# Kernel tuning notes

Measured on AMD Instinct MI355X. Metric: run time of the kernel, lower is better.

## Reference

```python
import jax, jax.numpy as jnp
import numpy as np

V, E, C, L, H, I = 50304, 512, 256, 6, 8, 1024
D = C // H            # head_dim = 32
ROT = int(D * 0.25)   # rotary_ndims = 8
B, S = 4, 1024


def _ln(x, w, b, eps=1e-5):
    m = x.mean(-1, keepdims=True)
    v = ((x - m) ** 2).mean(-1, keepdims=True)
    return (x - m) * jax.lax.rsqrt(v + eps) * w + b


def _apply_rope(x, cos, sin):
    # x: [B,S,H,D]; GPT-NeoX partial rotary on first ROT dims
    xr, xp = x[..., :ROT], x[..., ROT:]
    half = ROT // 2
    xrh = jnp.concatenate([-xr[..., half:], xr[..., :half]], -1)
    return jnp.concatenate([xr * cos + xrh * sin, xp], -1)


def setup_inputs() -> dict:
    key = jax.random.key(0)
    ks = jax.random.split(key, 16)
    std = 0.02
    inp = {
        'input_ids': jax.random.randint(ks[0], (B, S), 0, V),
        'prev_context': jnp.zeros((B, C), jnp.float32),
        'embed_w': jax.random.normal(ks[1], (V, E)) * std,
        'en_w': jnp.ones((E,)), 'en_b': jnp.zeros((E,)),
        # ContextBlock: Linear(context_dim+embed_dim -> context_dim) + GELU + LayerNorm
        'ctx_w': jax.random.normal(ks[2], (C, C + E)) * std,
        'ctx_b': jnp.zeros((C,)),
        'cn_w': jnp.ones((C,)), 'cn_b': jnp.zeros((C,)),
        # stacked per-layer Pythia params [L, ...]
        'ln1_w': jnp.ones((L, C)), 'ln1_b': jnp.zeros((L, C)),
        'ln2_w': jnp.ones((L, C)), 'ln2_b': jnp.zeros((L, C)),
        'qkv_w': jax.random.normal(ks[3], (L, 3 * C, C)) * std,
        'qkv_b': jnp.zeros((L, 3 * C)),
        'ao_w': jax.random.normal(ks[4], (L, C, C)) * std,
        'ao_b': jnp.zeros((L, C)),
        'fc1_w': jax.random.normal(ks[5], (L, I, C)) * std,
        'fc1_b': jnp.zeros((L, I)),
        'fc2_w': jax.random.normal(ks[6], (L, C, I)) * std,
        'fc2_b': jnp.zeros((L, C)),
        'fln_w': jnp.ones((C,)), 'fln_b': jnp.zeros((C,)),
        'out_w': jax.random.normal(ks[7], (V, C)) * std,
    }
    return inp


def reference(input_ids, prev_context, embed_w, en_w, en_b, ctx_w, ctx_b, cn_w, cn_b,
              ln1_w, ln1_b, ln2_w, ln2_b, qkv_w, qkv_b, ao_w, ao_b,
              fc1_w, fc1_b, fc2_w, fc2_b, fln_w, fln_b, out_w):
    b, s = input_ids.shape
    tok = _ln(embed_w[input_ids], en_w, en_b)                 # [B,S,E]

    # sequential context recurrence (scan == the per-token Python loop)
    def step(ctx, emb_t):
        h = jnp.concatenate([ctx, emb_t], -1) @ ctx_w.T + ctx_b
        ctx_new = _ln(jax.nn.gelu(h), cn_w, cn_b)
        return ctx_new, ctx_new
    _, hs = jax.lax.scan(step, prev_context, tok.transpose(1, 0, 2))
    x = hs.transpose(1, 0, 2)                                 # [B,S,C]

    pos = jnp.arange(s)
    inv = 1.0 / (10000.0 ** (jnp.arange(0, ROT, 2, dtype=jnp.float32) / ROT))
    ang = pos[:, None] * inv                                  # [S, ROT/2]
    cos = jnp.tile(jnp.cos(ang), (1, 2))[None, :, None, :]
    sin = jnp.tile(jnp.sin(ang), (1, 2))[None, :, None, :]
    causal = jnp.tril(jnp.ones((s, s), bool))

    for l in range(L):
        # parallel residual Pythia/GPT-NeoX layer
        a_in = _ln(x, ln1_w[l], ln1_b[l])
        qkv = jnp.einsum('bsc,oc->bso', a_in, qkv_w[l]) + qkv_b[l]
        q, k, v = [t.reshape(b, s, H, D) for t in jnp.split(qkv, 3, -1)]
        q = _apply_rope(q, cos, sin)
        k = _apply_rope(k, cos, sin)
        sc = jnp.einsum('bqhd,bkhd->bhqk', q, k) / jnp.sqrt(jnp.float32(D))
        sc = jnp.where(causal, sc, jnp.float32(-1e9))
        p = jax.nn.softmax(sc, -1)
        o = jnp.einsum('bhqk,bkhd->bqhd', p, v).reshape(b, s, C)
        attn = o @ ao_w[l].T + ao_b[l]
        m_in = _ln(x, ln2_w[l], ln2_b[l])
        mlp = jax.nn.gelu(m_in @ fc1_w[l].T + fc1_b[l]) @ fc2_w[l].T + fc2_b[l]
        x = x + attn + mlp

    x = _ln(x, fln_w, fln_b)
    logits = jnp.einsum('bsc,vc->bsv', x, out_w)              # [B,S,V]
    return logits
```

## Files before the change

kernel.cpp:

```cpp
#include <hip/hip_runtime.h>

typedef __bf16 bf16x8 __attribute__((ext_vector_type(8)));
typedef float  f32x4  __attribute__((ext_vector_type(4)));
typedef unsigned uint32x4 __attribute__((ext_vector_type(4)));

#define DEV __device__ __forceinline__

DEV ushort f2bf(float f) {
  unsigned u = __builtin_bit_cast(unsigned, f);
  u += 0x7FFFu + ((u >> 16) & 1u);
  return (ushort)(u >> 16);
}
DEV float bf2f(ushort u) { return __builtin_bit_cast(float, ((unsigned)u) << 16); }
DEV unsigned pk2(ushort a, ushort b) { return (unsigned)a | ((unsigned)b << 16); }

DEV f32x4 mfma16(bf16x8 a, bf16x8 b, f32x4 c) {
  return __builtin_amdgcn_mfma_f32_16x16x32_bf16(a, b, c, 0, 0, 0);
}

DEV float gelu_f(float x) {
  float u = 0.7978845608028654f * (x + 0.044715f * x * x * x);
  return x / (1.f + __expf(-2.f * u));
}

#define SEQ  1024
#define NBAT 4
#define CDIM 256
#define EDIM 512
#define NLAY 6
#define NHEAD 8
#define HDIM 32
#define IDIM 1024
#define NVOC 50304
#define NROWS (NBAT * SEQ)

__global__ __launch_bounds__(256) void cvt_k(const float* __restrict__ src,
                                             ushort* __restrict__ dst, int n4) {
  int i = blockIdx.x * blockDim.x + threadIdx.x;
  int stride = gridDim.x * blockDim.x;
  for (; i < n4; i += stride) {
    float4 f = ((const float4*)src)[i];
    ushort4 u; u.x = f2bf(f.x); u.y = f2bf(f.y); u.z = f2bf(f.z); u.w = f2bf(f.w);
    ((ushort4*)dst)[i] = u;
  }
}

__global__ __launch_bounds__(64) void embed_ln_k(const int* __restrict__ ids,
                                                 const float* __restrict__ ew,
                                                 const float* __restrict__ w,
                                                 const float* __restrict__ b,
                                                 ushort* __restrict__ tok) {
  int m = blockIdx.x, t = threadIdx.x;
  const float* row = ew + (size_t)ids[m] * EDIM;
  float4 v0 = *(const float4*)(row + t * 8);
  float4 v1 = *(const float4*)(row + t * 8 + 4);
  float sm = v0.x + v0.y + v0.z + v0.w + v1.x + v1.y + v1.z + v1.w;
  float sq = v0.x*v0.x + v0.y*v0.y + v0.z*v0.z + v0.w*v0.w
           + v1.x*v1.x + v1.y*v1.y + v1.z*v1.z + v1.w*v1.w;
#pragma unroll
  for (int msk = 1; msk <= 32; msk <<= 1) { sm += __shfl_xor(sm, msk); sq += __shfl_xor(sq, msk); }
  float mean = sm * (1.f / EDIM);
  float var  = sq * (1.f / EDIM) - mean * mean;
  float inv  = rsqrtf(var + 1e-5f);
  float4 w0 = *(const float4*)(w + t * 8), w1 = *(const float4*)(w + t * 8 + 4);
  float4 b0 = *(const float4*)(b + t * 8), b1 = *(const float4*)(b + t * 8 + 4);
  ushort4 u0, u1;
  u0.x = f2bf((v0.x - mean) * inv * w0.x + b0.x);
  u0.y = f2bf((v0.y - mean) * inv * w0.y + b0.y);
  u0.z = f2bf((v0.z - mean) * inv * w0.z + b0.z);
  u0.w = f2bf((v0.w - mean) * inv * w0.w + b0.w);
  u1.x = f2bf((v1.x - mean) * inv * w1.x + b1.x);
  u1.y = f2bf((v1.y - mean) * inv * w1.y + b1.y);
  u1.z = f2bf((v1.z - mean) * inv * w1.z + b1.z);
  u1.w = f2bf((v1.w - mean) * inv * w1.w + b1.w);
  *(ushort4*)(tok + (size_t)m * EDIM + t * 8)     = u0;
  *(ushort4*)(tok + (size_t)m * EDIM + t * 8 + 4) = u1;
}

template <bool DUAL>
__global__ __launch_bounds__(256) void ln_k(const float* __restrict__ x,
                                            const float* __restrict__ w1, const float* __restrict__ b1,
                                            const float* __restrict__ w2, const float* __restrict__ b2,
                                            ushort* __restrict__ o1, ushort* __restrict__ o2) {
  int wave = threadIdx.x >> 6, t = threadIdx.x & 63;
  int m = blockIdx.x * 4 + wave;
  const float* row = x + (size_t)m * CDIM;
  float4 v = *(const float4*)(row + t * 4);
  float sm = v.x + v.y + v.z + v.w;
  float sq = v.x*v.x + v.y*v.y + v.z*v.z + v.w*v.w;
#pragma unroll
  for (int msk = 1; msk <= 32; msk <<= 1) { sm += __shfl_xor(sm, msk); sq += __shfl_xor(sq, msk); }
  float mean = sm * (1.f / CDIM);
  float var  = sq * (1.f / CDIM) - mean * mean;
  float inv  = rsqrtf(var + 1e-5f);
  float n0 = (v.x - mean) * inv, n1 = (v.y - mean) * inv, n2 = (v.z - mean) * inv, n3 = (v.w - mean) * inv;
  {
    float4 wv = *(const float4*)(w1 + t * 4), bv = *(const float4*)(b1 + t * 4);
    ushort4 u; u.x = f2bf(n0*wv.x+bv.x); u.y = f2bf(n1*wv.y+bv.y); u.z = f2bf(n2*wv.z+bv.z); u.w = f2bf(n3*wv.w+bv.w);
    *(ushort4*)(o1 + (size_t)m * CDIM + t * 4) = u;
  }
  if constexpr (DUAL) {
    float4 wv = *(const float4*)(w2 + t * 4), bv = *(const float4*)(b2 + t * 4);
    ushort4 u; u.x = f2bf(n0*wv.x+bv.x); u.y = f2bf(n1*wv.y+bv.y); u.z = f2bf(n2*wv.z+bv.z); u.w = f2bf(n3*wv.w+bv.w);
    *(ushort4*)(o2 + (size_t)m * CDIM + t * 4) = u;
  }
}

enum { GF_BIAS = 1, GF_GELU = 2, GF_ACC = 4, GF_BF16O = 8, GF_WF32 = 16 };

template <int FLAGS>
__global__ __launch_bounds__(256) void gemm_k(const ushort* __restrict__ A, int lda,
                                              const void* __restrict__ Wv, int ldw,
                                              const float* __restrict__ bias,
                                              void* __restrict__ C, int ldc, int K) {
  __shared__ __attribute__((aligned(16))) ushort lsA[128 * 32];
  __shared__ __attribute__((aligned(16))) ushort lsB[128 * 32];
  const int tid = threadIdx.x, lane = tid & 63, wave = tid >> 6;
  const int wm = wave >> 1, wn = wave & 1;
  const int row0 = blockIdx.x * 128, col0 = blockIdx.y * 128;
  const int l15 = lane & 15, koff = (lane >> 4) * 8;

  f32x4 acc[4][4] = {};
  for (int k0 = 0; k0 < K; k0 += 32) {
    __syncthreads();
#pragma unroll
    for (int p = 0; p < 2; ++p) {
      int c = tid + p * 256;
      int r = c >> 2, k8 = (c & 3) * 8;
      *(uint4*)(&lsA[c * 8]) = *(const uint4*)(A + (size_t)(row0 + r) * lda + k0 + k8);
      if constexpr (FLAGS & GF_WF32) {
        const float* gw = (const float*)Wv + (size_t)(col0 + r) * ldw + k0 + k8;
        float4 f0 = *(const float4*)gw, f1 = *(const float4*)(gw + 4);
        uint4 vw;
        vw.x = pk2(f2bf(f0.x), f2bf(f0.y)); vw.y = pk2(f2bf(f0.z), f2bf(f0.w));
        vw.z = pk2(f2bf(f1.x), f2bf(f1.y)); vw.w = pk2(f2bf(f1.z), f2bf(f1.w));
        *(uint4*)(&lsB[c * 8]) = vw;
      } else {
        *(uint4*)(&lsB[c * 8]) = *(const uint4*)((const ushort*)Wv + (size_t)(col0 + r) * ldw + k0 + k8);
      }
    }
    __syncthreads();
    bf16x8 af[4], bfr[4];
#pragma unroll
    for (int mt = 0; mt < 4; ++mt)
      af[mt] = __builtin_bit_cast(bf16x8, *(const uint4*)(&lsA[(wm * 64 + mt * 16 + l15) * 32 + koff]));
#pragma unroll
    for (int nt = 0; nt < 4; ++nt)
      bfr[nt] = __builtin_bit_cast(bf16x8, *(const uint4*)(&lsB[(wn * 64 + nt * 16 + l15) * 32 + koff]));
#pragma unroll
    for (int mt = 0; mt < 4; ++mt)
#pragma unroll
      for (int nt = 0; nt < 4; ++nt)
        acc[mt][nt] = mfma16(af[mt], bfr[nt], acc[mt][nt]);
  }
#pragma unroll
  for (int mt = 0; mt < 4; ++mt) {
#pragma unroll
    for (int nt = 0; nt < 4; ++nt) {
      int col = col0 + wn * 64 + nt * 16 + l15;
      float bv = (FLAGS & GF_BIAS) ? bias[col] : 0.f;
      int rowb = row0 + wm * 64 + mt * 16 + (lane >> 4) * 4;
#pragma unroll
      for (int r = 0; r < 4; ++r) {
        float v = acc[mt][nt][r] + bv;
        if constexpr (FLAGS & GF_GELU) v = gelu_f(v);
        size_t off = (size_t)(rowb + r) * ldc + col;
        if constexpr (FLAGS & GF_ACC)        ((float*)C)[off] += v;
        else if constexpr (FLAGS & GF_BF16O) ((ushort*)C)[off] = f2bf(v);
        else                                 ((float*)C)[off] = v;
      }
    }
  }
}

template <int FLAGS>
__global__ __launch_bounds__(256) void gemm64_k(const ushort* __restrict__ A, int lda,
                                                const void* __restrict__ Wv, int ldw,
                                                const float* __restrict__ bias,
                                                void* __restrict__ C, int ldc, int K) {
  __shared__ __attribute__((aligned(16))) ushort lsA[64 * 32];
  __shared__ __attribute__((aligned(16))) ushort lsB[64 * 32];
  const int tid = threadIdx.x, lane = tid & 63, wave = tid >> 6;
  const int row0 = blockIdx.x * 64, col0 = blockIdx.y * 64;
  const int l15 = lane & 15, lhi = lane >> 4, koff = lhi * 8;

  f32x4 acc[4] = {};
  for (int k0 = 0; k0 < K; k0 += 32) {
    __syncthreads();
    {
      int r = tid >> 2, k8 = (tid & 3) * 8;
      *(uint4*)(&lsA[tid * 8]) = *(const uint4*)(A + (size_t)(row0 + r) * lda + k0 + k8);
      if constexpr (FLAGS & GF_WF32) {
        const float* gw = (const float*)Wv + (size_t)(col0 + r) * ldw + k0 + k8;
        float4 f0 = *(const float4*)gw, f1 = *(const float4*)(gw + 4);
        uint4 vw;
        vw.x = pk2(f2bf(f0.x), f2bf(f0.y)); vw.y = pk2(f2bf(f0.z), f2bf(f0.w));
        vw.z = pk2(f2bf(f1.x), f2bf(f1.y)); vw.w = pk2(f2bf(f1.z), f2bf(f1.w));
        *(uint4*)(&lsB[tid * 8]) = vw;
      } else {
        *(uint4*)(&lsB[tid * 8]) = *(const uint4*)((const ushort*)Wv + (size_t)(col0 + r) * ldw + k0 + k8);
      }
    }
    __syncthreads();
    bf16x8 af = __builtin_bit_cast(bf16x8, *(const uint4*)(&lsA[(wave * 16 + l15) * 32 + koff]));
#pragma unroll
    for (int nt = 0; nt < 4; ++nt) {
      bf16x8 bfr = __builtin_bit_cast(bf16x8, *(const uint4*)(&lsB[(nt * 16 + l15) * 32 + koff]));
      acc[nt] = mfma16(af, bfr, acc[nt]);
    }
  }
#pragma unroll
  for (int nt = 0; nt < 4; ++nt) {
    int col = col0 + nt * 16 + l15;
    float bv = (FLAGS & GF_BIAS) ? bias[col] : 0.f;
    int rowb = row0 + wave * 16 + lhi * 4;
#pragma unroll
    for (int r = 0; r < 4; ++r) {
      float v = acc[nt][r] + bv;
      if constexpr (FLAGS & GF_GELU) v = gelu_f(v);
      size_t off = (size_t)(rowb + r) * ldc + col;
      if constexpr (FLAGS & GF_ACC)        ((float*)C)[off] += v;
      else if constexpr (FLAGS & GF_BF16O) ((ushort*)C)[off] = f2bf(v);
      else                                 ((float*)C)[off] = v;
    }
  }
}

__global__ __launch_bounds__(512, 2) void scan_k(const float* __restrict__ ctx_w,
                                                 const float* __restrict__ prev_ctx,
                                                 const float* __restrict__ P,
                                                 const float* __restrict__ cn_w,
                                                 const float* __restrict__ cn_b,
                                                 float* __restrict__ x) {
  __shared__ __attribute__((aligned(16))) ushort g_lds[2][4 * 288];
  __shared__ __attribute__((aligned(16))) float  part_lds[2][4][8][2];
  const int tid = threadIdx.x, lane = tid & 63, wave = tid >> 6;
  const int l15 = lane & 15, lhi = lane >> 4;
  const int bb = l15 & 3;
  const int ss = l15 >> 2;
  const int mt = ss & 1, rp = ss >> 1;
  const int c0 = wave * 32 + mt * 16 + lhi * 4 + rp * 2;

  float2 wv  = *(const float2*)(cn_w + c0);
  float2 bv2 = *(const float2*)(cn_b + c0);
  float s1v0 = 0.f, s1v1 = 0.f, c1v0 = 0.f, c1v1 = 0.f;
#pragma unroll 1
  for (int kk = 0; kk < CDIM; kk += 4) {
    float4 wk = *(const float4*)(cn_w + kk);
    float4 bk = *(const float4*)(cn_b + kk);
    float4 W0 = *(const float4*)(ctx_w + (size_t)c0 * 768 + kk);
    float4 W1 = *(const float4*)(ctx_w + (size_t)(c0 + 1) * 768 + kk);
    s1v0 += W0.x*wk.x + W0.y*wk.y + W0.z*wk.z + W0.w*wk.w;
    c1v0 += W0.x*bk.x + W0.y*bk.y + W0.z*bk.z + W0.w*bk.w;
    s1v1 += W1.x*wk.x + W1.y*wk.y + W1.z*wk.z + W1.w*wk.w;
    c1v1 += W1.x*bk.x + W1.y*bk.y + W1.z*bk.z + W1.w*bk.w;
  }

  {
    float2 c2 = *(const float2*)(prev_ctx + bb * CDIM + c0);
    ushort2 u; u.x = f2bf(c2.x); u.y = f2bf(c2.y);
    *(ushort2*)&g_lds[0][bb * 288 + c0] = u;
  }

  uint32x4 wfu[2][8];
#pragma unroll
  for (int m2 = 0; m2 < 2; ++m2)
#pragma unroll
    for (int kt = 0; kt < 8; ++kt) {
      const float* s = ctx_w + (size_t)(wave * 32 + m2 * 16 + l15) * 768 + kt * 32 + lhi * 8;
      float4 f0 = *(const float4*)s, f1 = *(const float4*)(s + 4);
      uint32x4 vw;
      vw.x = pk2(f2bf(f0.x), f2bf(f0.y)); vw.y = pk2(f2bf(f0.z), f2bf(f0.w));
      vw.z = pk2(f2bf(f1.x), f2bf(f1.y)); vw.w = pk2(f2bf(f1.z), f2bf(f1.w));
      wfu[m2][kt] = vw;
    }
  float2 pf  = *(const float2*)(P + ((size_t)bb * SEQ + 0) * CDIM + c0);
  float2 pn1 = *(const float2*)(P + ((size_t)bb * SEQ + 1) * CDIM + c0);
  float2 pn2 = *(const float2*)(P + ((size_t)bb * SEQ + 2) * CDIM + c0);
  __syncthreads();

  float gr[2];
  {
    uint32x4 bfr[8];
#pragma unroll
    for (int kt = 0; kt < 8; ++kt)
      bfr[kt] = *(const uint32x4*)(&g_lds[0][bb * 288 + kt * 32 + lhi * 8]);
    f32x4 acc[2] = {};
#pragma unroll
    for (int m2 = 0; m2 < 2; ++m2)
#pragma unroll
      for (int kt = 0; kt < 8; ++kt)
        acc[m2] = mfma16(__builtin_bit_cast(bf16x8, wfu[m2][kt]),
                         __builtin_bit_cast(bf16x8, bfr[kt]), acc[m2]);
    f32x4 av = (mt == 0) ? acc[0] : acc[1];
    gr[0] = gelu_f(av[rp * 2]     + pf.x);
    gr[1] = gelu_f(av[rp * 2 + 1] + pf.y);
  }

#pragma unroll
  for (int m2 = 0; m2 < 2; ++m2)
#pragma unroll
    for (int kt = 0; kt < 8; ++kt) {
      int k = kt * 32 + lhi * 8;
      const float* s = ctx_w + (size_t)(wave * 32 + m2 * 16 + l15) * 768 + k;
      float4 f0 = *(const float4*)s, f1 = *(const float4*)(s + 4);
      float4 w0 = *(const float4*)(cn_w + k), w1 = *(const float4*)(cn_w + k + 4);
      uint32x4 vw;
      vw.x = pk2(f2bf(f0.x * w0.x), f2bf(f0.y * w0.y));
      vw.y = pk2(f2bf(f0.z * w0.z), f2bf(f0.w * w0.w));
      vw.z = pk2(f2bf(f1.x * w1.x), f2bf(f1.y * w1.y));
      vw.w = pk2(f2bf(f1.z * w1.z), f2bf(f1.w * w1.w));
      wfu[m2][kt] = vw;
    }
#pragma unroll
  for (int m2 = 0; m2 < 2; ++m2)
#pragma unroll
    for (int kt = 0; kt < 8; ++kt)
      asm volatile("" : "+v"(wfu[m2][kt]));
  pf = pn1; pn1 = pn2;
  pn2 = *(const float2*)(P + ((size_t)bb * SEQ + 3) * CDIM + c0);
  __syncthreads();

  {
    ushort2 u; u.x = f2bf(gr[0]); u.y = f2bf(gr[1]);
    *(ushort2*)&g_lds[0][bb * 288 + c0] = u;
    float lsm = gr[0] + gr[1];
    float lsq = gr[0]*gr[0] + gr[1]*gr[1];
    lsm += __shfl_xor(lsm, 4);  lsq += __shfl_xor(lsq, 4);
    lsm += __shfl_xor(lsm, 8);  lsq += __shfl_xor(lsq, 8);
    lsm += __shfl_xor(lsm, 16); lsq += __shfl_xor(lsq, 16);
    lsm += __shfl_xor(lsm, 32); lsq += __shfl_xor(lsq, 32);
    if (ss == 0 && lhi == 0) {
      float2 pq; pq.x = lsm; pq.y = lsq;
      *(float2*)&part_lds[0][l15][wave][0] = pq;
    }
  }
  __syncthreads();

  for (int t = 0; t < SEQ; ++t) {
    const int cur = t & 1, nxt = cur ^ 1;
    int tp = (t + 4 < SEQ) ? t + 4 : SEQ - 1;
    float2 pl = *(const float2*)(P + ((size_t)bb * SEQ + tp) * CDIM + c0);

    uint32x4 bfr[8];
#pragma unroll
    for (int kt = 0; kt < 8; ++kt)
      bfr[kt] = *(const uint32x4*)(&g_lds[cur][bb * 288 + kt * 32 + lhi * 8]);
    const float4* pp = (const float4*)&part_lds[cur][bb][0][0];
    float4 qa = pp[0], qb = pp[1], qc = pp[2], qd = pp[3];

    f32x4 accA[2] = {}, accB[2] = {};
#pragma unroll
    for (int m2 = 0; m2 < 2; ++m2) {
      accA[m2] = mfma16(__builtin_bit_cast(bf16x8, wfu[m2][0]), __builtin_bit_cast(bf16x8, bfr[0]), accA[m2]);
      accB[m2] = mfma16(__builtin_bit_cast(bf16x8, wfu[m2][4]), __builtin_bit_cast(bf16x8, bfr[4]), accB[m2]);
      accA[m2] = mfma16(__builtin_bit_cast(bf16x8, wfu[m2][1]), __builtin_bit_cast(bf16x8, bfr[1]), accA[m2]);
      accB[m2] = mfma16(__builtin_bit_cast(bf16x8, wfu[m2][5]), __builtin_bit_cast(bf16x8, bfr[5]), accB[m2]);
      accA[m2] = mfma16(__builtin_bit_cast(bf16x8, wfu[m2][2]), __builtin_bit_cast(bf16x8, bfr[2]), accA[m2]);
      accB[m2] = mfma16(__builtin_bit_cast(bf16x8, wfu[m2][6]), __builtin_bit_cast(bf16x8, bfr[6]), accB[m2]);
      accA[m2] = mfma16(__builtin_bit_cast(bf16x8, wfu[m2][3]), __builtin_bit_cast(bf16x8, bfr[3]), accA[m2]);
      accB[m2] = mfma16(__builtin_bit_cast(bf16x8, wfu[m2][7]), __builtin_bit_cast(bf16x8, bfr[7]), accB[m2]);
    }

    float sm = (qa.x + qa.z) + (qb.x + qb.z) + (qc.x + qc.z) + (qd.x + qd.z);
    float sq = (qa.y + qa.w) + (qb.y + qb.w) + (qc.y + qc.w) + (qd.y + qd.w);
    float mu  = sm * (1.f / CDIM);
    float inv = rsqrtf(sq * (1.f / CDIM) - mu * mu + 1e-5f);
    float invmu = inv * mu;

    float2 y;
    y.x = wv.x * (inv * gr[0] - invmu) + bv2.x;
    y.y = wv.y * (inv * gr[1] - invmu) + bv2.y;
    *(float2*)(x + ((size_t)bb * SEQ + t) * CDIM + c0) = y;

    f32x4 avA = (mt == 0) ? accA[0] : accA[1];
    f32x4 avB = (mt == 0) ? accB[0] : accB[1];
    float a0 = avA[rp * 2]     + avB[rp * 2];
    float a1 = avA[rp * 2 + 1] + avB[rp * 2 + 1];
    gr[0] = gelu_f(inv * a0 - invmu * s1v0 + c1v0 + pf.x);
    gr[1] = gelu_f(inv * a1 - invmu * s1v1 + c1v1 + pf.y);
    {
      ushort2 u; u.x = f2bf(gr[0]); u.y = f2bf(gr[1]);
      *(ushort2*)&g_lds[nxt][bb * 288 + c0] = u;
    }
    float lsm = gr[0] + gr[1];
    float lsq = gr[0]*gr[0] + gr[1]*gr[1];
    lsm += __shfl_xor(lsm, 4);  lsq += __shfl_xor(lsq, 4);
    lsm += __shfl_xor(lsm, 8);  lsq += __shfl_xor(lsq, 8);
    lsm += __shfl_xor(lsm, 16); lsq += __shfl_xor(lsq, 16);
    lsm += __shfl_xor(lsm, 32); lsq += __shfl_xor(lsq, 32);
    if (ss == 0 && lhi == 0) {
      float2 pq; pq.x = lsm; pq.y = lsq;
      *(float2*)&part_lds[nxt][l15][wave][0] = pq;
    }
    pf = pn1; pn1 = pn2; pn2 = pl;
    asm volatile("s_waitcnt lgkmcnt(0)" ::: "memory");
    __builtin_amdgcn_s_barrier();
    __builtin_amdgcn_sched_barrier(0);
  }
}

__global__ __launch_bounds__(256) void rope_k(const ushort* __restrict__ qkv,
                                              ushort* __restrict__ Qo,
                                              ushort* __restrict__ Ko,
                                              ushort* __restrict__ Vt) {
  int m = blockIdx.x;
  int b = m >> 10, s = m & 1023;
  int t = threadIdx.x;
  int h = t >> 5, d = t & 31;
  const ushort* row = qkv + (size_t)m * 768;
  float q = bf2f(row[h * 32 + d]);
  float k = bf2f(row[256 + h * 32 + d]);
  float v = bf2f(row[512 + h * 32 + d]);
  if (d < 8) {
    int prt = (d < 4) ? d + 4 : d - 4;
    float sgn = (d < 4) ? -1.f : 1.f;
    float qp = sgn * bf2f(row[h * 32 + prt]);
    float kp = sgn * bf2f(row[256 + h * 32 + prt]);
    int j = d & 3;
    const float invs[4] = {1.f, 0.1f, 0.01f, 0.001f};
    float ang = (float)s * invs[j];
    float c, sn;
    __sincosf(ang, &sn, &c);
    q = q * c + qp * sn;
    k = k * c + kp * sn;
  }
  size_t bh = (size_t)(b * NHEAD + h);
  Qo[(bh * SEQ + s) * HDIM + d] = f2bf(q);
  Ko[(bh * SEQ + s) * HDIM + d] = f2bf(k);
  Vt[bh * HDIM * SEQ + (size_t)d * SEQ + s] = f2bf(v);
}

__global__ __launch_bounds__(256) void attn_k(const ushort* __restrict__ Q,
                                              const ushort* __restrict__ K,
                                              const ushort* __restrict__ VT,
                                              ushort* __restrict__ O) {
  __shared__ __attribute__((aligned(16))) ushort Plds[4 * 16 * 32];
  const int tid = threadIdx.x, lane = tid & 63, wave = tid >> 6;
  const int bh = blockIdx.y;
  const int qtile = blockIdx.x * 4 + wave;
  const int q0 = qtile * 16;
  const int l15 = lane & 15, lhi = lane >> 4;
  const float scale = 0.17677669529663689f;

  bf16x8 qa = __builtin_bit_cast(bf16x8,
      *(const uint4*)(Q + ((size_t)bh * SEQ + q0 + l15) * HDIM + lhi * 8));
  const ushort* Kb = K + (size_t)bh * SEQ * HDIM;
  const ushort* Vb = VT + (size_t)bh * HDIM * SEQ;
  ushort* Pw = &Plds[wave * 512];

  f32x4 o0 = {}, o1 = {};
  float lacc[4] = {};

  for (int kt = 0; kt <= qtile; kt += 2) {
    const bool t2 = (kt + 1 <= qtile);
    f32x4 z = {};
    bf16x8 kf0 = __builtin_bit_cast(bf16x8, *(const uint4*)(Kb + (size_t)(kt * 16 + l15) * HDIM + lhi * 8));
    f32x4 s0 = mfma16(qa, kf0, z);
    f32x4 s1 = {};
    if (t2) {
      bf16x8 kf1 = __builtin_bit_cast(bf16x8, *(const uint4*)(Kb + (size_t)((kt + 1) * 16 + l15) * HDIM + lhi * 8));
      s1 = mfma16(qa, kf1, z);
    }
    float p0[4], p1[4];
#pragma unroll
    for (int r = 0; r < 4; ++r) {
      int qr = q0 + lhi * 4 + r;
      int kc0 = kt * 16 + l15;
      p0[r] = (kc0 <= qr) ? __expf(s0[r] * scale) : 0.f;
      p1[r] = (t2 && kc0 + 16 <= qr) ? __expf(s1[r] * scale) : 0.f;
      lacc[r] += p0[r] + p1[r];
    }
#pragma unroll
    for (int r = 0; r < 4; ++r) {
      Pw[(lhi * 4 + r) * 32 + l15]      = f2bf(p0[r]);
      Pw[(lhi * 4 + r) * 32 + 16 + l15] = f2bf(p1[r]);
    }
    bf16x8 pa  = __builtin_bit_cast(bf16x8, *(const uint4*)(&Pw[l15 * 32 + lhi * 8]));
    bf16x8 v0f = __builtin_bit_cast(bf16x8, *(const uint4*)(Vb + (size_t)l15 * SEQ + kt * 16 + lhi * 8));
    bf16x8 v1f = __builtin_bit_cast(bf16x8, *(const uint4*)(Vb + (size_t)(16 + l15) * SEQ + kt * 16 + lhi * 8));
    o0 = mfma16(pa, v0f, o0);
    o1 = mfma16(pa, v1f, o1);
  }
#pragma unroll
  for (int msk = 1; msk <= 8; msk <<= 1)
#pragma unroll
    for (int r = 0; r < 4; ++r) lacc[r] += __shfl_xor(lacc[r], msk);

  const int b = bh >> 3, h = bh & 7;
#pragma unroll
  for (int r = 0; r < 4; ++r) {
    float inv = 1.f / lacc[r];
    int qr = q0 + lhi * 4 + r;
    size_t base = ((size_t)(b * SEQ + qr)) * CDIM + h * HDIM;
    O[base + l15]      = f2bf(o0[r] * inv);
    O[base + 16 + l15] = f2bf(o1[r] * inv);
  }
}

static size_t ws_take(size_t& o, size_t bytes) {
  size_t r = o;
  o += (bytes + 255) & ~(size_t)255;
  return r;
}

extern "C" void kernel_launch(void* const* d_in, const int* in_sizes, int n_in,
                              void* d_out, int out_size, void* d_ws, size_t ws_size,
                              hipStream_t stream) {
  (void)in_sizes; (void)n_in; (void)out_size; (void)ws_size;
  const int*   input_ids = (const int*)  d_in[0];
  const float* prev_ctx  = (const float*)d_in[1];
  const float* embed_w   = (const float*)d_in[2];
  const float* en_w      = (const float*)d_in[3];
  const float* en_b      = (const float*)d_in[4];
  const float* ctx_w     = (const float*)d_in[5];
  const float* ctx_b     = (const float*)d_in[6];
  const float* cn_w      = (const float*)d_in[7];
  const float* cn_b      = (const float*)d_in[8];
  const float* ln1_w     = (const float*)d_in[9];
  const float* ln1_b     = (const float*)d_in[10];
  const float* ln2_w     = (const float*)d_in[11];
  const float* ln2_b     = (const float*)d_in[12];
  const float* qkv_w     = (const float*)d_in[13];
  const float* qkv_b     = (const float*)d_in[14];
  const float* ao_w      = (const float*)d_in[15];
  const float* ao_b      = (const float*)d_in[16];
  const float* fc1_w     = (const float*)d_in[17];
  const float* fc1_b     = (const float*)d_in[18];
  const float* fc2_w     = (const float*)d_in[19];
  const float* fc2_b     = (const float*)d_in[20];
  const float* fln_w     = (const float*)d_in[21];
  const float* fln_b     = (const float*)d_in[22];
  const float* out_w     = (const float*)d_in[23];
  float* logits = (float*)d_out;

  char* ws = (char*)d_ws;
  size_t o = 0;
  ushort* WB_OUT = (ushort*)(ws + ws_take(o, (size_t)NVOC * CDIM * 2));
  ushort* TOK    = (ushort*)(ws + ws_take(o, (size_t)NROWS * EDIM * 2));
  float*  PBUF   = (float*) (ws + ws_take(o, (size_t)NROWS * CDIM * 4));
  float*  XBUF   = (float*) (ws + ws_take(o, (size_t)NROWS * CDIM * 4));
  ushort* AIN    = (ushort*)(ws + ws_take(o, (size_t)NROWS * CDIM * 2));
  ushort* MIN    = (ushort*)(ws + ws_take(o, (size_t)NROWS * CDIM * 2));
  ushort* QKVB   = (ushort*)(ws + ws_take(o, (size_t)NROWS * 768 * 2));
  ushort* QB     = (ushort*)(ws + ws_take(o, (size_t)NROWS * CDIM * 2));
  ushort* KB     = (ushort*)(ws + ws_take(o, (size_t)NROWS * CDIM * 2));
  ushort* VTB    = (ushort*)(ws + ws_take(o, (size_t)NROWS * CDIM * 2));
  ushort* OB     = (ushort*)(ws + ws_take(o, (size_t)NROWS * CDIM * 2));
  ushort* TBUF   = (ushort*)(ws + ws_take(o, (size_t)NROWS * IDIM * 2));
  ushort* XLN    = (ushort*)(ws + ws_take(o, (size_t)NROWS * CDIM * 2));

  cvt_k<<<dim3(2048), dim3(256), 0, stream>>>(out_w, WB_OUT, NVOC * CDIM / 4);
  embed_ln_k<<<dim3(NROWS), dim3(64), 0, stream>>>(input_ids, embed_w, en_w, en_b, TOK);
  gemm64_k<GF_BIAS | GF_WF32><<<dim3(64, 4), dim3(256), 0, stream>>>(
      TOK, EDIM, (const void*)(ctx_w + 256), 768, ctx_b, (void*)PBUF, CDIM, EDIM);
  scan_k<<<dim3(1), dim3(512), 0, stream>>>(ctx_w, prev_ctx, PBUF, cn_w, cn_b, XBUF);

  for (int l = 0; l < NLAY; ++l) {
    ln_k<true><<<dim3(NROWS / 4), dim3(256), 0, stream>>>(
        XBUF, ln1_w + l * CDIM, ln1_b + l * CDIM, ln2_w + l * CDIM, ln2_b + l * CDIM, AIN, MIN);
    gemm64_k<GF_BIAS | GF_BF16O | GF_WF32><<<dim3(64, 12), dim3(256), 0, stream>>>(
        AIN, CDIM, (const void*)(qkv_w + (size_t)l * 768 * CDIM), CDIM,
        qkv_b + l * 768, (void*)QKVB, 768, CDIM);
    rope_k<<<dim3(NROWS), dim3(256), 0, stream>>>(QKVB, QB, KB, VTB);
    attn_k<<<dim3(16, 32), dim3(256), 0, stream>>>(QB, KB, VTB, OB);
    gemm64_k<GF_BIAS | GF_ACC | GF_WF32><<<dim3(64, 4), dim3(256), 0, stream>>>(
        OB, CDIM, (const void*)(ao_w + (size_t)l * CDIM * CDIM), CDIM,
        ao_b + l * CDIM, (void*)XBUF, CDIM, CDIM);
    gemm64_k<GF_BIAS | GF_GELU | GF_BF16O | GF_WF32><<<dim3(64, 16), dim3(256), 0, stream>>>(
        MIN, CDIM, (const void*)(fc1_w + (size_t)l * IDIM * CDIM), CDIM,
        fc1_b + l * IDIM, (void*)TBUF, IDIM, CDIM);
    gemm64_k<GF_BIAS | GF_ACC | GF_WF32><<<dim3(64, 4), dim3(256), 0, stream>>>(
        TBUF, IDIM, (const void*)(fc2_w + (size_t)l * CDIM * IDIM), IDIM,
        fc2_b + l * CDIM, (void*)XBUF, CDIM, IDIM);
  }

  ln_k<false><<<dim3(NROWS / 4), dim3(256), 0, stream>>>(
      XBUF, fln_w, fln_b, nullptr, nullptr, XLN, nullptr);
  gemm_k<0><<<dim3(32, 393), dim3(256), 0, stream>>>(
      XLN, CDIM, (const void*)WB_OUT, CDIM, nullptr, (void*)logits, NVOC, CDIM);
}
```

Measured before the change: 2.020 ms.

## Fuse RoPE into QKV GEMM, merge attn-out and FC2 GEMMs, restructure scan

Three independent changes. RoPE is folded into the QKV GEMM epilogue, using a lane shuffle to fetch the rotary partner, so the intermediate QKV buffer and the separate rope kernel go away. The attention-output and FC2 projections become one dual-K GEMM that accumulates into the residual once, removing a launch and one read-modify-write of X per layer. The sequential scan kernel drops from 8 to 4 waves, with each lane owning 4 columns, and is unrolled by 4 so the prefetch registers rotate statically; the aim is shorter per-step barrier and reduction cost on the serial critical path, at the price of more MFMA work per wave.

Result: faster. 1.805 ms (-10.6%).

```diff
diff --git a/kernel.cpp b/kernel.cpp
--- a/kernel.cpp
+++ b/kernel.cpp
@@ -226,83 +226,199 @@
   }
 }
 
-__global__ __launch_bounds__(512, 2) void scan_k(const float* __restrict__ ctx_w,
+__global__ __launch_bounds__(256) void qkvrope_k(const ushort* __restrict__ A,
+                                                 const float* __restrict__ W,
+                                                 const float* __restrict__ bias,
+                                                 ushort* __restrict__ Qo,
+                                                 ushort* __restrict__ Ko,
+                                                 ushort* __restrict__ Vt) {
+  __shared__ __attribute__((aligned(16))) ushort lsA[64 * 32];
+  __shared__ __attribute__((aligned(16))) ushort lsB[64 * 32];
+  const int tid = threadIdx.x, lane = tid & 63, wave = tid >> 6;
+  const int row0 = blockIdx.x * 64, col0 = blockIdx.y * 64;
+  const int l15 = lane & 15, lhi = lane >> 4, koff = lhi * 8;
+
+  f32x4 acc[4] = {};
+  for (int k0 = 0; k0 < CDIM; k0 += 32) {
+    __syncthreads();
+    {
+      int r = tid >> 2, k8 = (tid & 3) * 8;
+      *(uint4*)(&lsA[tid * 8]) = *(const uint4*)(A + (size_t)(row0 + r) * CDIM + k0 + k8);
+      const float* gw = W + (size_t)(col0 + r) * CDIM + k0 + k8;
+      float4 f0 = *(const float4*)gw, f1 = *(const float4*)(gw + 4);
+      uint4 vw;
+      vw.x = pk2(f2bf(f0.x), f2bf(f0.y)); vw.y = pk2(f2bf(f0.z), f2bf(f0.w));
+      vw.z = pk2(f2bf(f1.x), f2bf(f1.y)); vw.w = pk2(f2bf(f1.z), f2bf(f1.w));
+      *(uint4*)(&lsB[tid * 8]) = vw;
+    }
+    __syncthreads();
+    bf16x8 af = __builtin_bit_cast(bf16x8, *(const uint4*)(&lsA[(wave * 16 + l15) * 32 + koff]));
+#pragma unroll
+    for (int nt = 0; nt < 4; ++nt) {
+      bf16x8 bfr = __builtin_bit_cast(bf16x8, *(const uint4*)(&lsB[(nt * 16 + l15) * 32 + koff]));
+      acc[nt] = mfma16(af, bfr, acc[nt]);
+    }
+  }
+  const int rowb = row0 + wave * 16 + lhi * 4;
+  const int b = rowb >> 10, s0 = rowb & 1023;
+#pragma unroll
+  for (int nt = 0; nt < 4; ++nt) {
+    int c = col0 + nt * 16 + l15;
+    int which = c >> 8;
+    int h = (c >> 5) & 7;
+    int d = c & 31;
+    size_t bh = (size_t)(b * NHEAD + h);
+    float bv = bias[c];
+    float val[4], part[4];
+#pragma unroll
+    for (int r = 0; r < 4; ++r) val[r] = acc[nt][r] + bv;
+#pragma unroll
+    for (int r = 0; r < 4; ++r) part[r] = __shfl_xor(val[r], 4);
+    if (d < 8 && which < 2) {
+      float sgn = (d < 4) ? -1.f : 1.f;
+      int j = d & 3;
+      float invp = (j == 0) ? 1.f : (j == 1) ? 0.1f : (j == 2) ? 0.01f : 0.001f;
+#pragma unroll
+      for (int r = 0; r < 4; ++r) {
+        float ang = (float)(s0 + r) * invp;
+        float cs, sn;
+        __sincosf(ang, &sn, &cs);
+        val[r] = val[r] * cs + sgn * part[r] * sn;
+      }
+    }
+    if (which == 2) {
+      ushort4 u; u.x = f2bf(val[0]); u.y = f2bf(val[1]); u.z = f2bf(val[2]); u.w = f2bf(val[3]);
+      *(ushort4*)(Vt + bh * HDIM * SEQ + (size_t)d * SEQ + s0) = u;
+    } else {
+      ushort* dst = (which == 0) ? Qo : Ko;
+#pragma unroll
+      for (int r = 0; r < 4; ++r)
+        dst[(bh * SEQ + s0 + r) * HDIM + d] = f2bf(val[r]);
+    }
+  }
+}
+
+__global__ __launch_bounds__(256) void gemm64_dual_k(const ushort* __restrict__ A1, int lda1,
+                                                     const float* __restrict__ W1, int ldw1, int K1,
+                                                     const ushort* __restrict__ A2, int lda2,
+                                                     const float* __restrict__ W2, int ldw2, int K2,
+                                                     const float* __restrict__ b1,
+                                                     const float* __restrict__ b2,
+                                                     float* __restrict__ C, int ldc) {
+  __shared__ __attribute__((aligned(16))) ushort lsA[64 * 32];
+  __shared__ __attribute__((aligned(16))) ushort lsB[64 * 32];
+  const int tid = threadIdx.x, lane = tid & 63, wave = tid >> 6;
+  const int row0 = blockIdx.x * 64, col0 = blockIdx.y * 64;
+  const int l15 = lane & 15, lhi = lane >> 4, koff = lhi * 8;
+
+  f32x4 acc[4] = {};
+  for (int k0 = 0; k0 < K1 + K2; k0 += 32) {
+    __syncthreads();
+    {
+      int r = tid >> 2, k8 = (tid & 3) * 8;
+      const ushort* Ap; const float* Wp; int kk;
+      if (k0 < K1) { Ap = A1 + (size_t)(row0 + r) * lda1; Wp = W1 + (size_t)(col0 + r) * ldw1; kk = k0 + k8; }
+      else         { Ap = A2 + (size_t)(row0 + r) * lda2; Wp = W2 + (size_t)(col0 + r) * ldw2; kk = k0 - K1 + k8; }
+      *(uint4*)(&lsA[tid * 8]) = *(const uint4*)(Ap + kk);
+      float4 f0 = *(const float4*)(Wp + kk), f1 = *(const float4*)(Wp + kk + 4);
+      uint4 vw;
+      vw.x = pk2(f2bf(f0.x), f2bf(f0.y)); vw.y = pk2(f2bf(f0.z), f2bf(f0.w));
+      vw.z = pk2(f2bf(f1.x), f2bf(f1.y)); vw.w = pk2(f2bf(f1.z), f2bf(f1.w));
+      *(uint4*)(&lsB[tid * 8]) = vw;
+    }
+    __syncthreads();
+    bf16x8 af = __builtin_bit_cast(bf16x8, *(const uint4*)(&lsA[(wave * 16 + l15) * 32 + koff]));
+#pragma unroll
+    for (int nt = 0; nt < 4; ++nt) {
+      bf16x8 bfr = __builtin_bit_cast(bf16x8, *(const uint4*)(&lsB[(nt * 16 + l15) * 32 + koff]));
+      acc[nt] = mfma16(af, bfr, acc[nt]);
+    }
+  }
+#pragma unroll
+  for (int nt = 0; nt < 4; ++nt) {
+    int col = col0 + nt * 16 + l15;
+    float bv = b1[col] + b2[col];
+    int rowb = row0 + wave * 16 + lhi * 4;
+#pragma unroll
+    for (int r = 0; r < 4; ++r)
+      C[(size_t)(rowb + r) * ldc + col] += acc[nt][r] + bv;
+  }
+}
+
+__global__ __launch_bounds__(256, 1) void scan_k(const float* __restrict__ ctx_w,
                                                  const float* __restrict__ prev_ctx,
                                                  const float* __restrict__ P,
                                                  const float* __restrict__ cn_w,
                                                  const float* __restrict__ cn_b,
                                                  float* __restrict__ x) {
   __shared__ __attribute__((aligned(16))) ushort g_lds[2][4 * 288];
-  __shared__ __attribute__((aligned(16))) float  part_lds[2][4][8][2];
+  __shared__ __attribute__((aligned(16))) float  part_lds[2][4][4][2];
   const int tid = threadIdx.x, lane = tid & 63, wave = tid >> 6;
   const int l15 = lane & 15, lhi = lane >> 4;
   const int bb = l15 & 3;
   const int ss = l15 >> 2;
-  const int mt = ss & 1, rp = ss >> 1;
-  const int c0 = wave * 32 + mt * 16 + lhi * 4 + rp * 2;
-
-  float2 wv  = *(const float2*)(cn_w + c0);
-  float2 bv2 = *(const float2*)(cn_b + c0);
-  float s1v0 = 0.f, s1v1 = 0.f, c1v0 = 0.f, c1v1 = 0.f;
+  const int ccol = wave * 64 + ss * 16 + lhi * 4;
+
+  float4 wv  = *(const float4*)(cn_w + ccol);
+  float4 bvv = *(const float4*)(cn_b + ccol);
+  float s1v[4] = {}, c1v[4] = {};
 #pragma unroll 1
   for (int kk = 0; kk < CDIM; kk += 4) {
     float4 wk = *(const float4*)(cn_w + kk);
     float4 bk = *(const float4*)(cn_b + kk);
-    float4 W0 = *(const float4*)(ctx_w + (size_t)c0 * 768 + kk);
-    float4 W1 = *(const float4*)(ctx_w + (size_t)(c0 + 1) * 768 + kk);
-    s1v0 += W0.x*wk.x + W0.y*wk.y + W0.z*wk.z + W0.w*wk.w;
-    c1v0 += W0.x*bk.x + W0.y*bk.y + W0.z*bk.z + W0.w*bk.w;
-    s1v1 += W1.x*wk.x + W1.y*wk.y + W1.z*wk.z + W1.w*wk.w;
-    c1v1 += W1.x*bk.x + W1.y*bk.y + W1.z*bk.z + W1.w*bk.w;
+#pragma unroll
+    for (int j = 0; j < 4; ++j) {
+      float4 Wr = *(const float4*)(ctx_w + (size_t)(ccol + j) * 768 + kk);
+      s1v[j] += Wr.x * wk.x + Wr.y * wk.y + Wr.z * wk.z + Wr.w * wk.w;
+      c1v[j] += Wr.x * bk.x + Wr.y * bk.y + Wr.z * bk.z + Wr.w * bk.w;
+    }
   }
 
   {
-    float2 c2 = *(const float2*)(prev_ctx + bb * CDIM + c0);
-    ushort2 u; u.x = f2bf(c2.x); u.y = f2bf(c2.y);
-    *(ushort2*)&g_lds[0][bb * 288 + c0] = u;
-  }
-
-  uint32x4 wfu[2][8];
-#pragma unroll
-  for (int m2 = 0; m2 < 2; ++m2)
+    float4 c4 = *(const float4*)(prev_ctx + bb * CDIM + ccol);
+    ushort4 u; u.x = f2bf(c4.x); u.y = f2bf(c4.y); u.z = f2bf(c4.z); u.w = f2bf(c4.w);
+    *(ushort4*)&g_lds[0][bb * 288 + ccol] = u;
+  }
+
+  uint32x4 wfu[4][8];
+#pragma unroll
+  for (int mt = 0; mt < 4; ++mt)
 #pragma unroll
     for (int kt = 0; kt < 8; ++kt) {
-      const float* s = ctx_w + (size_t)(wave * 32 + m2 * 16 + l15) * 768 + kt * 32 + lhi * 8;
+      const float* s = ctx_w + (size_t)(wave * 64 + mt * 16 + l15) * 768 + kt * 32 + lhi * 8;
       float4 f0 = *(const float4*)s, f1 = *(const float4*)(s + 4);
       uint32x4 vw;
       vw.x = pk2(f2bf(f0.x), f2bf(f0.y)); vw.y = pk2(f2bf(f0.z), f2bf(f0.w));
       vw.z = pk2(f2bf(f1.x), f2bf(f1.y)); vw.w = pk2(f2bf(f1.z), f2bf(f1.w));
-      wfu[m2][kt] = vw;
-    }
-  float2 pf  = *(const float2*)(P + ((size_t)bb * SEQ + 0) * CDIM + c0);
-  float2 pn1 = *(const float2*)(P + ((size_t)bb * SEQ + 1) * CDIM + c0);
-  float2 pn2 = *(const float2*)(P + ((size_t)bb * SEQ + 2) * CDIM + c0);
+      wfu[mt][kt] = vw;
+    }
+  float4 pf = *(const float4*)(P + ((size_t)bb * SEQ + 0) * CDIM + ccol);
   __syncthreads();
 
-  float gr[2];
+  float gr[4];
   {
     uint32x4 bfr[8];
 #pragma unroll
     for (int kt = 0; kt < 8; ++kt)
       bfr[kt] = *(const uint32x4*)(&g_lds[0][bb * 288 + kt * 32 + lhi * 8]);
-    f32x4 acc[2] = {};
-#pragma unroll
-    for (int m2 = 0; m2 < 2; ++m2)
+    f32x4 acc[4] = {};
+#pragma unroll
+    for (int mt = 0; mt < 4; ++mt)
 #pragma unroll
       for (int kt = 0; kt < 8; ++kt)
-        acc[m2] = mfma16(__builtin_bit_cast(bf16x8, wfu[m2][kt]),
-                         __builtin_bit_cast(bf16x8, bfr[kt]), acc[m2]);
-    f32x4 av = (mt == 0) ? acc[0] : acc[1];
-    gr[0] = gelu_f(av[rp * 2]     + pf.x);
-    gr[1] = gelu_f(av[rp * 2 + 1] + pf.y);
-  }
-
-#pragma unroll
-  for (int m2 = 0; m2 < 2; ++m2)
+        acc[mt] = mfma16(__builtin_bit_cast(bf16x8, wfu[mt][kt]),
+                         __builtin_bit_cast(bf16x8, bfr[kt]), acc[mt]);
+    f32x4 av = (ss == 0) ? acc[0] : (ss == 1) ? acc[1] : (ss == 2) ? acc[2] : acc[3];
+    gr[0] = gelu_f(av[0] + pf.x); gr[1] = gelu_f(av[1] + pf.y);
+    gr[2] = gelu_f(av[2] + pf.z); gr[3] = gelu_f(av[3] + pf.w);
+  }
+
+#pragma unroll
+  for (int mt = 0; mt < 4; ++mt)
 #pragma unroll
     for (int kt = 0; kt < 8; ++kt) {
       int k = kt * 32 + lhi * 8;
-      const float* s = ctx_w + (size_t)(wave * 32 + m2 * 16 + l15) * 768 + k;
+      const float* s = ctx_w + (size_t)(wave * 64 + mt * 16 + l15) * 768 + k;
       float4 f0 = *(const float4*)s, f1 = *(const float4*)(s + 4);
       float4 w0 = *(const float4*)(cn_w + k), w1 = *(const float4*)(cn_w + k + 4);
       uint32x4 vw;
@@ -310,125 +426,103 @@
       vw.y = pk2(f2bf(f0.z * w0.z), f2bf(f0.w * w0.w));
       vw.z = pk2(f2bf(f1.x * w1.x), f2bf(f1.y * w1.y));
       vw.w = pk2(f2bf(f1.z * w1.z), f2bf(f1.w * w1.w));
-      wfu[m2][kt] = vw;
-    }
-#pragma unroll
-  for (int m2 = 0; m2 < 2; ++m2)
+      wfu[mt][kt] = vw;
+    }
+#pragma unroll
+  for (int mt = 0; mt < 4; ++mt)
 #pragma unroll
     for (int kt = 0; kt < 8; ++kt)
-      asm volatile("" : "+v"(wfu[m2][kt]));
-  pf = pn1; pn1 = pn2;
-  pn2 = *(const float2*)(P + ((size_t)bb * SEQ + 3) * CDIM + c0);
+      asm volatile("" : "+v"(wfu[mt][kt]));
+
+  float4 ps0, ps1, ps2, ps3;
+  ps1 = *(const float4*)(P + ((size_t)bb * SEQ + 1) * CDIM + ccol);
+  ps2 = *(const float4*)(P + ((size_t)bb * SEQ + 2) * CDIM + ccol);
+  ps3 = *(const float4*)(P + ((size_t)bb * SEQ + 3) * CDIM + ccol);
+  ps0 = ps3;
   __syncthreads();
 
   {
-    ushort2 u; u.x = f2bf(gr[0]); u.y = f2bf(gr[1]);
-    *(ushort2*)&g_lds[0][bb * 288 + c0] = u;
-    float lsm = gr[0] + gr[1];
-    float lsq = gr[0]*gr[0] + gr[1]*gr[1];
+    ushort4 u; u.x = f2bf(gr[0]); u.y = f2bf(gr[1]); u.z = f2bf(gr[2]); u.w = f2bf(gr[3]);
+    *(ushort4*)&g_lds[0][bb * 288 + ccol] = u;
+    float lsm = gr[0] + gr[1] + gr[2] + gr[3];
+    float lsq = gr[0]*gr[0] + gr[1]*gr[1] + gr[2]*gr[2] + gr[3]*gr[3];
     lsm += __shfl_xor(lsm, 4);  lsq += __shfl_xor(lsq, 4);
     lsm += __shfl_xor(lsm, 8);  lsq += __shfl_xor(lsq, 8);
     lsm += __shfl_xor(lsm, 16); lsq += __shfl_xor(lsq, 16);
     lsm += __shfl_xor(lsm, 32); lsq += __shfl_xor(lsq, 32);
     if (ss == 0 && lhi == 0) {
-      float2 pq; pq.x = lsm; pq.y = lsq;
-      *(float2*)&part_lds[0][l15][wave][0] = pq;
+      part_lds[0][bb][wave][0] = lsm;
+      part_lds[0][bb][wave][1] = lsq;
     }
   }
   __syncthreads();
 
-  for (int t = 0; t < SEQ; ++t) {
-    const int cur = t & 1, nxt = cur ^ 1;
-    int tp = (t + 4 < SEQ) ? t + 4 : SEQ - 1;
-    float2 pl = *(const float2*)(P + ((size_t)bb * SEQ + tp) * CDIM + c0);
-
-    uint32x4 bfr[8];
-#pragma unroll
-    for (int kt = 0; kt < 8; ++kt)
-      bfr[kt] = *(const uint32x4*)(&g_lds[cur][bb * 288 + kt * 32 + lhi * 8]);
-    const float4* pp = (const float4*)&part_lds[cur][bb][0][0];
-    float4 qa = pp[0], qb = pp[1], qc = pp[2], qd = pp[3];
-
-    f32x4 accA[2] = {}, accB[2] = {};
-#pragma unroll
-    for (int m2 = 0; m2 < 2; ++m2) {
-      accA[m2] = mfma16(__builtin_bit_cast(bf16x8, wfu[m2][0]), __builtin_bit_cast(bf16x8, bfr[0]), accA[m2]);
-      accB[m2] = mfma16(__builtin_bit_cast(bf16x8, wfu[m2][4]), __builtin_bit_cast(bf16x8, bfr[4]), accB[m2]);
-      accA[m2] = mfma16(__builtin_bit_cast(bf16x8, wfu[m2][1]), __builtin_bit_cast(bf16x8, bfr[1]), accA[m2]);
-      accB[m2] = mfma16(__builtin_bit_cast(bf16x8, wfu[m2][5]), __builtin_bit_cast(bf16x8, bfr[5]), accB[m2]);
-      accA[m2] = mfma16(__builtin_bit_cast(bf16x8, wfu[m2][2]), __builtin_bit_cast(bf16x8, bfr[2]), accA[m2]);
-      accB[m2] = mfma16(__builtin_bit_cast(bf16x8, wfu[m2][6]), __builtin_bit_cast(bf16x8, bfr[6]), accB[m2]);
-      accA[m2] = mfma16(__builtin_bit_cast(bf16x8, wfu[m2][3]), __builtin_bit_cast(bf16x8, bfr[3]), accA[m2]);
-      accB[m2] = mfma16(__builtin_bit_cast(bf16x8, wfu[m2][7]), __builtin_bit_cast(bf16x8, bfr[7]), accB[m2]);
-    }
-
-    float sm = (qa.x + qa.z) + (qb.x + qb.z) + (qc.x + qc.z) + (qd.x + qd.z);
-    float sq = (qa.y + qa.w) + (qb.y + qb.w) + (qc.y + qc.w) + (qd.y + qd.w);
-    float mu  = sm * (1.f / CDIM);
-    float inv = rsqrtf(sq * (1.f / CDIM) - mu * mu + 1e-5f);
-    float invmu = inv * mu;
-
-    float2 y;
-    y.x = wv.x * (inv * gr[0] - invmu) + bv2.x;
-    y.y = wv.y * (inv * gr[1] - invmu) + bv2.y;
-    *(float2*)(x + ((size_t)bb * SEQ + t) * CDIM + c0) = y;
-
-    f32x4 avA = (mt == 0) ? accA[0] : accA[1];
-    f32x4 avB = (mt == 0) ? accB[0] : accB[1];
-    float a0 = avA[rp * 2]     + avB[rp * 2];
-    float a1 = avA[rp * 2 + 1] + avB[rp * 2 + 1];
-    gr[0] = gelu_f(inv * a0 - invmu * s1v0 + c1v0 + pf.x);
-    gr[1] = gelu_f(inv * a1 - invmu * s1v1 + c1v1 + pf.y);
-    {
-      ushort2 u; u.x = f2bf(gr[0]); u.y = f2bf(gr[1]);
-      *(ushort2*)&g_lds[nxt][bb * 288 + c0] = u;
-    }
-    float lsm = gr[0] + gr[1];
-    float lsq = gr[0]*gr[0] + gr[1]*gr[1];
-    lsm += __shfl_xor(lsm, 4);  lsq += __shfl_xor(lsq, 4);
-    lsm += __shfl_xor(lsm, 8);  lsq += __shfl_xor(lsq, 8);
-    lsm += __shfl_xor(lsm, 16); lsq += __shfl_xor(lsq, 16);
-    lsm += __shfl_xor(lsm, 32); lsq += __shfl_xor(lsq, 32);
-    if (ss == 0 && lhi == 0) {
-      float2 pq; pq.x = lsm; pq.y = lsq;
-      *(float2*)&part_lds[nxt][l15][wave][0] = pq;
-    }
-    pf = pn1; pn1 = pn2; pn2 = pl;
-    asm volatile("s_waitcnt lgkmcnt(0)" ::: "memory");
-    __builtin_amdgcn_s_barrier();
-    __builtin_amdgcn_sched_barrier(0);
-  }
-}
-
-__global__ __launch_bounds__(256) void rope_k(const ushort* __restrict__ qkv,
-                                              ushort* __restrict__ Qo,
-                                              ushort* __restrict__ Ko,
-                                              ushort* __restrict__ Vt) {
-  int m = blockIdx.x;
-  int b = m >> 10, s = m & 1023;
-  int t = threadIdx.x;
-  int h = t >> 5, d = t & 31;
-  const ushort* row = qkv + (size_t)m * 768;
-  float q = bf2f(row[h * 32 + d]);
-  float k = bf2f(row[256 + h * 32 + d]);
-  float v = bf2f(row[512 + h * 32 + d]);
-  if (d < 8) {
-    int prt = (d < 4) ? d + 4 : d - 4;
-    float sgn = (d < 4) ? -1.f : 1.f;
-    float qp = sgn * bf2f(row[h * 32 + prt]);
-    float kp = sgn * bf2f(row[256 + h * 32 + prt]);
-    int j = d & 3;
-    const float invs[4] = {1.f, 0.1f, 0.01f, 0.001f};
-    float ang = (float)s * invs[j];
-    float c, sn;
-    __sincosf(ang, &sn, &c);
-    q = q * c + qp * sn;
-    k = k * c + kp * sn;
-  }
-  size_t bh = (size_t)(b * NHEAD + h);
-  Qo[(bh * SEQ + s) * HDIM + d] = f2bf(q);
-  Ko[(bh * SEQ + s) * HDIM + d] = f2bf(k);
-  Vt[bh * HDIM * SEQ + (size_t)d * SEQ + s] = f2bf(v);
+#define SCAN_STEP(T, CUR, NXT, PUSE, PLOAD)                                          \
+  {                                                                                  \
+    int tp = ((T) + 4 < SEQ) ? (T) + 4 : SEQ - 1;                                    \
+    PLOAD = *(const float4*)(P + ((size_t)bb * SEQ + tp) * CDIM + ccol);             \
+    uint32x4 bfr[8];                                                                 \
+    _Pragma("unroll")                                                                \
+    for (int kt = 0; kt < 8; ++kt)                                                   \
+      bfr[kt] = *(const uint32x4*)(&g_lds[CUR][bb * 288 + kt * 32 + lhi * 8]);       \
+    const float4* pp = (const float4*)&part_lds[CUR][bb][0][0];                      \
+    float4 qpa = pp[0], qpb = pp[1];                                                 \
+    f32x4 accA[4] = {}, accB[4] = {};                                                \
+    _Pragma("unroll")                                                                \
+    for (int mt = 0; mt < 4; ++mt) {                                                 \
+      accA[mt] = mfma16(__builtin_bit_cast(bf16x8, wfu[mt][0]), __builtin_bit_cast(bf16x8, bfr[0]), accA[mt]); \
+      accB[mt] = mfma16(__builtin_bit_cast(bf16x8, wfu[mt][4]), __builtin_bit_cast(bf16x8, bfr[4]), accB[mt]); \
+      accA[mt] = mfma16(__builtin_bit_cast(bf16x8, wfu[mt][1]), __builtin_bit_cast(bf16x8, bfr[1]), accA[mt]); \
+      accB[mt] = mfma16(__builtin_bit_cast(bf16x8, wfu[mt][5]), __builtin_bit_cast(bf16x8, bfr[5]), accB[mt]); \
+      accA[mt] = mfma16(__builtin_bit_cast(bf16x8, wfu[mt][2]), __builtin_bit_cast(bf16x8, bfr[2]), accA[mt]); \
+      accB[mt] = mfma16(__builtin_bit_cast(bf16x8, wfu[mt][6]), __builtin_bit_cast(bf16x8, bfr[6]), accB[mt]); \
+      accA[mt] = mfma16(__builtin_bit_cast(bf16x8, wfu[mt][3]), __builtin_bit_cast(bf16x8, bfr[3]), accA[mt]); \
+      accB[mt] = mfma16(__builtin_bit_cast(bf16x8, wfu[mt][7]), __builtin_bit_cast(bf16x8, bfr[7]), accB[mt]); \
+    }                                                                                \
+    float sm = (qpa.x + qpa.z) + (qpb.x + qpb.z);                                    \
+    float sq = (qpa.y + qpa.w) + (qpb.y + qpb.w);                                    \
+    float mu  = sm * (1.f / CDIM);                                                   \
+    float inv = rsqrtf(sq * (1.f / CDIM) - mu * mu + 1e-5f);                         \
+    float invmu = inv * mu;                                                          \
+    float4 y;                                                                        \
+    y.x = wv.x * (inv * gr[0] - invmu) + bvv.x;                                      \
+    y.y = wv.y * (inv * gr[1] - invmu) + bvv.y;                                      \
+    y.z = wv.z * (inv * gr[2] - invmu) + bvv.z;                                      \
+    y.w = wv.w * (inv * gr[3] - invmu) + bvv.w;                                      \
+    *(float4*)(x + ((size_t)bb * SEQ + (T)) * CDIM + ccol) = y;                      \
+    f32x4 avA = (ss == 0) ? accA[0] : (ss == 1) ? accA[1] : (ss == 2) ? accA[2] : accA[3]; \
+    f32x4 avB = (ss == 0) ? accB[0] : (ss == 1) ? accB[1] : (ss == 2) ? accB[2] : accB[3]; \
+    f32x4 av = avA + avB;                                                            \
+    gr[0] = gelu_f(inv * av[0] - invmu * s1v[0] + c1v[0] + PUSE.x);                  \
+    gr[1] = gelu_f(inv * av[1] - invmu * s1v[1] + c1v[1] + PUSE.y);                  \
+    gr[2] = gelu_f(inv * av[2] - invmu * s1v[2] + c1v[2] + PUSE.z);                  \
+    gr[3] = gelu_f(inv * av[3] - invmu * s1v[3] + c1v[3] + PUSE.w);                  \
+    {                                                                                \
+      ushort4 u; u.x = f2bf(gr[0]); u.y = f2bf(gr[1]); u.z = f2bf(gr[2]); u.w = f2bf(gr[3]); \
+      *(ushort4*)&g_lds[NXT][bb * 288 + ccol] = u;                                   \
+    }                                                                                \
+    float lsm = gr[0] + gr[1] + gr[2] + gr[3];                                       \
+    float lsq = gr[0]*gr[0] + gr[1]*gr[1] + gr[2]*gr[2] + gr[3]*gr[3];               \
+    lsm += __shfl_xor(lsm, 4);  lsq += __shfl_xor(lsq, 4);                           \
+    lsm += __shfl_xor(lsm, 8);  lsq += __shfl_xor(lsq, 8);                           \
+    lsm += __shfl_xor(lsm, 16); lsq += __shfl_xor(lsq, 16);                          \
+    lsm += __shfl_xor(lsm, 32); lsq += __shfl_xor(lsq, 32);                          \
+    if (ss == 0 && lhi == 0) {                                                       \
+      part_lds[NXT][bb][wave][0] = lsm;                                              \
+      part_lds[NXT][bb][wave][1] = lsq;                                              \
+    }                                                                                \
+    asm volatile("s_waitcnt lgkmcnt(0)" ::: "memory");                               \
+    __builtin_amdgcn_s_barrier();                                                    \
+    __builtin_amdgcn_sched_barrier(0);                                               \
+  }
+
+  for (int t = 0; t < SEQ; t += 4) {
+    SCAN_STEP(t,     0, 1, ps1, ps0)
+    SCAN_STEP(t + 1, 1, 0, ps2, ps1)
+    SCAN_STEP(t + 2, 0, 1, ps3, ps2)
+    SCAN_STEP(t + 3, 1, 0, ps0, ps3)
+  }
+#undef SCAN_STEP
 }
 
 __global__ __launch_bounds__(256) void attn_k(const ushort* __restrict__ Q,
@@ -542,7 +636,6 @@
   float*  XBUF   = (float*) (ws + ws_take(o, (size_t)NROWS * CDIM * 4));
   ushort* AIN    = (ushort*)(ws + ws_take(o, (size_t)NROWS * CDIM * 2));
   ushort* MIN    = (ushort*)(ws + ws_take(o, (size_t)NROWS * CDIM * 2));
-  ushort* QKVB   = (ushort*)(ws + ws_take(o, (size_t)NROWS * 768 * 2));
   ushort* QB     = (ushort*)(ws + ws_take(o, (size_t)NROWS * CDIM * 2));
   ushort* KB     = (ushort*)(ws + ws_take(o, (size_t)NROWS * CDIM * 2));
   ushort* VTB    = (ushort*)(ws + ws_take(o, (size_t)NROWS * CDIM * 2));
@@ -554,25 +647,21 @@
   embed_ln_k<<<dim3(NROWS), dim3(64), 0, stream>>>(input_ids, embed_w, en_w, en_b, TOK);
   gemm64_k<GF_BIAS | GF_WF32><<<dim3(64, 4), dim3(256), 0, stream>>>(
       TOK, EDIM, (const void*)(ctx_w + 256), 768, ctx_b, (void*)PBUF, CDIM, EDIM);
-  scan_k<<<dim3(1), dim3(512), 0, stream>>>(ctx_w, prev_ctx, PBUF, cn_w, cn_b, XBUF);
+  scan_k<<<dim3(1), dim3(256), 0, stream>>>(ctx_w, prev_ctx, PBUF, cn_w, cn_b, XBUF);
 
   for (int l = 0; l < NLAY; ++l) {
     ln_k<true><<<dim3(NROWS / 4), dim3(256), 0, stream>>>(
         XBUF, ln1_w + l * CDIM, ln1_b + l * CDIM, ln2_w + l * CDIM, ln2_b + l * CDIM, AIN, MIN);
-    gemm64_k<GF_BIAS | GF_BF16O | GF_WF32><<<dim3(64, 12), dim3(256), 0, stream>>>(
-        AIN, CDIM, (const void*)(qkv_w + (size_t)l * 768 * CDIM), CDIM,
-        qkv_b + l * 768, (void*)QKVB, 768, CDIM);
-    rope_k<<<dim3(NROWS), dim3(256), 0, stream>>>(QKVB, QB, KB, VTB);
+    qkvrope_k<<<dim3(64, 12), dim3(256), 0, stream>>>(
+        AIN, qkv_w + (size_t)l * 768 * CDIM, qkv_b + l * 768, QB, KB, VTB);
     attn_k<<<dim3(16, 32), dim3(256), 0, stream>>>(QB, KB, VTB, OB);
-    gemm64_k<GF_BIAS | GF_ACC | GF_WF32><<<dim3(64, 4), dim3(256), 0, stream>>>(
-        OB, CDIM, (const void*)(ao_w + (size_t)l * CDIM * CDIM), CDIM,
-        ao_b + l * CDIM, (void*)XBUF, CDIM, CDIM);
     gemm64_k<GF_BIAS | GF_GELU | GF_BF16O | GF_WF32><<<dim3(64, 16), dim3(256), 0, stream>>>(
         MIN, CDIM, (const void*)(fc1_w + (size_t)l * IDIM * CDIM), CDIM,
         fc1_b + l * IDIM, (void*)TBUF, IDIM, CDIM);
-    gemm64_k<GF_BIAS | GF_ACC | GF_WF32><<<dim3(64, 4), dim3(256), 0, stream>>>(
-        TBUF, IDIM, (const void*)(fc2_w + (size_t)l * CDIM * IDIM), IDIM,
-        fc2_b + l * CDIM, (void*)XBUF, CDIM, IDIM);
+    gemm64_dual_k<<<dim3(64, 4), dim3(256), 0, stream>>>(
+        OB, CDIM, ao_w + (size_t)l * CDIM * CDIM, CDIM, CDIM,
+        TBUF, IDIM, fc2_w + (size_t)l * CDIM * IDIM, IDIM, IDIM,
+        ao_b + l * CDIM, fc2_b + l * CDIM, XBUF, CDIM);
   }
 
   ln_k<false><<<dim3(NROWS / 4), dim3(256), 0, stream>>>(
```
